# Optimization experiments

Hardware: AMD Instinct MI355X
Metric: run time of the kernel (lower is better)

## Reference

```python
import jax, jax.numpy as jnp
import numpy as np

D = 256  # out_size / d_model
B, S = 8, 4096


def setup_inputs() -> dict:
    key = jax.random.key(0)
    ks = jax.random.split(key, 10)
    std = 1.0 / np.sqrt(D)
    x = jax.random.normal(ks[0], (B, S, D), dtype=jnp.float32)
    Wq = jax.random.uniform(ks[1], (D, D), jnp.float32, -std, std)
    bq = jax.random.uniform(ks[2], (D,), jnp.float32, -std, std)
    Wk = jax.random.uniform(ks[3], (D, D), jnp.float32, -std, std)
    bk = jax.random.uniform(ks[4], (D,), jnp.float32, -std, std)
    Wv = jax.random.uniform(ks[5], (D, D), jnp.float32, -std, std)
    bv = jax.random.uniform(ks[6], (D,), jnp.float32, -std, std)
    Wo = jax.random.uniform(ks[7], (D, D), jnp.float32, -std, std)
    bo = jax.random.uniform(ks[8], (D,), jnp.float32, -std, std)
    cv = jax.random.normal(ks[9], (D, 1), dtype=jnp.float32)
    return {"x": x, "Wq": Wq, "bq": bq, "Wk": Wk, "bk": bk,
            "Wv": Wv, "bv": bv, "Wo": Wo, "bo": bo, "cv": cv}


def reference(x, Wq, bq, Wk, bk, Wv, bv, Wo, bo, cv):
    # Local single-head attention: separate matmul / softmax / matmul
    q = jnp.einsum('bsd,de->bse', x, Wq) + bq
    k = jnp.einsum('bsd,de->bse', x, Wk) + bk
    v = jnp.einsum('bsd,de->bse', x, Wv) + bv
    scale = jnp.sqrt(jnp.asarray(D, dtype=x.dtype))
    scores = jnp.einsum('bqd,bkd->bqk', q, k) / scale  # [B,S,S]
    attn = jax.nn.softmax(scores, axis=-1)
    ctx = jnp.einsum('bqk,bkd->bqd', attn, v)
    logits = jnp.einsum('bsd,de->bse', ctx, Wo) + bo
    # Global context-vector pooling weights (softmax over sequence dim)
    w = jnp.einsum('bsd,dk->bsk', logits, cv)          # [B,S,1]
    nw = jax.nn.softmax(w, axis=1)
    return logits * nw
```

## Files before the change

kernel.cpp:

```cpp
#include <hip/hip_runtime.h>
#include <math.h>
#include <cstddef>
#include <cstdint>

#define B_ 8
#define S_ 4096
#define D_ 256

typedef __attribute__((ext_vector_type(8))) short short8v;
typedef __attribute__((ext_vector_type(4))) short short4v;
typedef __attribute__((ext_vector_type(4))) float float4v;

__device__ __forceinline__ unsigned short f2bf(float f) {
  unsigned u = __float_as_uint(f);
  return (unsigned short)((u + 0x7FFF + ((u >> 16) & 1)) >> 16);
}
__device__ __forceinline__ float bf2f(unsigned short h) {
  return __uint_as_float((unsigned)h << 16);
}
__device__ __forceinline__ unsigned packp(float p) {
  const unsigned short hh = f2bf(p);
  const unsigned short ll = f2bf(p - bf2f(hh));
  return ((unsigned)hh << 16) | (unsigned)ll;
}

__global__ __launch_bounds__(256) void wsplit_kernel(
    const float* __restrict__ Wq, const float* __restrict__ Wk,
    const float* __restrict__ Wv, const float* __restrict__ Wo,
    short* __restrict__ wsp) {
  const int mat = blockIdx.x >> 4;
  const int k0  = (blockIdx.x & 15) << 4;
  const float* W = (mat == 0) ? Wq : (mat == 1) ? Wk : (mat == 2) ? Wv : Wo;
  const int n = threadIdx.x;
  short8v h0, h1, l0, l1;
#pragma unroll
  for (int j = 0; j < 8; ++j) {
    float y = W[(size_t)(k0 + j) * 256 + n];
    unsigned short hh = f2bf(y);
    h0[j] = (short)hh; l0[j] = (short)f2bf(y - bf2f(hh));
    y = W[(size_t)(k0 + 8 + j) * 256 + n];
    hh = f2bf(y);
    h1[j] = (short)hh; l1[j] = (short)f2bf(y - bf2f(hh));
  }
  short* dh = wsp + (size_t)mat * 131072 + (size_t)n * 256 + k0;
  short* dl = dh + 65536;
  *(short8v*)(dh + 0) = h0; *(short8v*)(dh + 8) = h1;
  *(short8v*)(dl + 0) = l0; *(short8v*)(dl + 8) = l1;
}

__global__ __launch_bounds__(256, 2) void proj_qkv_mfma(
    const float* __restrict__ x, const short* __restrict__ wsp,
    const float* __restrict__ bq, const float* __restrict__ bk,
    const float* __restrict__ bvv,
    short* __restrict__ qh, short* __restrict__ ql,
    short* __restrict__ kh, short* __restrict__ kl,
    short* __restrict__ vth, short* __restrict__ vtl) {
  __shared__ __align__(16) short sWh[256 * 40];
  __shared__ __align__(16) short sWl[256 * 40];

  const int t    = threadIdx.x;
  const int w    = t >> 6;
  const int lane = t & 63;
  const int m    = lane & 15;
  const int quad = lane >> 4;
  const size_t r0 = (size_t)blockIdx.x * 64;
  const size_t srow = r0 + 16 * w + m;

  short8v xh[8], xl[8];
#pragma unroll
  for (int kk = 0; kk < 8; ++kk) {
    const float* xp = x + srow * 256 + kk * 32 + quad * 8;
    const float4 a = *(const float4*)xp;
    const float4 b2 = *(const float4*)(xp + 4);
    const float v[8] = {a.x, a.y, a.z, a.w, b2.x, b2.y, b2.z, b2.w};
    short8v h, l;
#pragma unroll
    for (int e = 0; e < 8; ++e) {
      const unsigned short hh = f2bf(v[e]);
      h[e] = (short)hh; l[e] = (short)f2bf(v[e] - bf2f(hh));
    }
    xh[kk] = h; xl[kk] = l;
  }

#pragma unroll
  for (int p = 0; p < 3; ++p) {
    const short* wbase = wsp + (size_t)p * 131072;
    float4v acc[16];
#pragma unroll
    for (int nt = 0; nt < 16; ++nt) acc[nt] = (float4v){0.f, 0.f, 0.f, 0.f};

    for (int kk = 0; kk < 8; ++kk) {
      __syncthreads();
      {
        const short* gh = wbase + (size_t)t * 256 + kk * 32;
        const short* gl = gh + 65536;
#pragma unroll
        for (int j = 0; j < 4; ++j) {
          *(short8v*)&sWh[t * 40 + j * 8] = *(const short8v*)(gh + j * 8);
          *(short8v*)&sWl[t * 40 + j * 8] = *(const short8v*)(gl + j * 8);
        }
      }
      __syncthreads();
#pragma unroll
      for (int nt = 0; nt < 16; ++nt) {
        const short8v wh = *(const short8v*)&sWh[(nt * 16 + m) * 40 + quad * 8];
        const short8v wl = *(const short8v*)&sWl[(nt * 16 + m) * 40 + quad * 8];
        if (p < 2) {
          acc[nt] = __builtin_amdgcn_mfma_f32_16x16x32_bf16(wh, xh[kk], acc[nt], 0, 0, 0);
          acc[nt] = __builtin_amdgcn_mfma_f32_16x16x32_bf16(wh, xl[kk], acc[nt], 0, 0, 0);
          acc[nt] = __builtin_amdgcn_mfma_f32_16x16x32_bf16(wl, xh[kk], acc[nt], 0, 0, 0);
        } else {
          acc[nt] = __builtin_amdgcn_mfma_f32_16x16x32_bf16(xh[kk], wh, acc[nt], 0, 0, 0);
          acc[nt] = __builtin_amdgcn_mfma_f32_16x16x32_bf16(xh[kk], wl, acc[nt], 0, 0, 0);
          acc[nt] = __builtin_amdgcn_mfma_f32_16x16x32_bf16(xl[kk], wh, acc[nt], 0, 0, 0);
        }
      }
    }

    if (p < 2) {
      const float scale = (p == 0) ? 0.0625f : 1.0f;
      short* oh = (p == 0) ? qh : kh;
      short* ol = (p == 0) ? ql : kl;
      const float* bias = (p == 0) ? bq : bk;
#pragma unroll
      for (int nt = 0; nt < 16; ++nt) {
        const float4 bb = *(const float4*)(bias + nt * 16 + quad * 4);
        const float bb4[4] = {bb.x, bb.y, bb.z, bb.w};
        short4v h4, l4;
#pragma unroll
        for (int r = 0; r < 4; ++r) {
          const float y = (acc[nt][r] + bb4[r]) * scale;
          const unsigned short hh = f2bf(y);
          h4[r] = (short)hh; l4[r] = (short)f2bf(y - bf2f(hh));
        }
        *(short4v*)(oh + srow * 256 + nt * 16 + quad * 4) = h4;
        *(short4v*)(ol + srow * 256 + nt * 16 + quad * 4) = l4;
      }
    } else {
      const int bidx = (int)(r0 >> 12);
      const size_t bD = (size_t)bidx * (D_ * (size_t)S_);
      const int sl0 = (int)(r0 & 4095) + 16 * w + quad * 4;
#pragma unroll
      for (int nt = 0; nt < 16; ++nt) {
        const int d = nt * 16 + m;
        const float bn = bvv[d];
        short4v h4, l4;
#pragma unroll
        for (int r = 0; r < 4; ++r) {
          const float y = acc[nt][r] + bn;
          const unsigned short hh = f2bf(y);
          h4[r] = (short)hh; l4[r] = (short)f2bf(y - bf2f(hh));
        }
        *(short4v*)(vth + bD + (size_t)d * S_ + sl0) = h4;
        *(short4v*)(vtl + bD + (size_t)d * S_ + sl0) = l4;
      }
    }
  }
}

__global__ __launch_bounds__(256, 2) void gemm_out_mfma(
    const float* __restrict__ ctx, const short* __restrict__ wsp,
    const float* __restrict__ bo, const float* __restrict__ cv,
    float* __restrict__ out, float* __restrict__ wvec) {
  __shared__ __align__(16) short sWh[256 * 40];
  __shared__ __align__(16) short sWl[256 * 40];

  const int t    = threadIdx.x;
  const int w    = t >> 6;
  const int lane = t & 63;
  const int m    = lane & 15;
  const int quad = lane >> 4;
  const size_t r0 = (size_t)blockIdx.x * 64;
  const size_t srow = r0 + 16 * w + m;
  const short* wbase = wsp + (size_t)3 * 131072;

  short8v ah[8], al[8];
#pragma unroll
  for (int kk = 0; kk < 8; ++kk) {
    const float* xp = ctx + srow * 256 + kk * 32 + quad * 8;
    const float4 a = *(const float4*)xp;
    const float4 b2 = *(const float4*)(xp + 4);
    const float v[8] = {a.x, a.y, a.z, a.w, b2.x, b2.y, b2.z, b2.w};
    short8v h, l;
#pragma unroll
    for (int e = 0; e < 8; ++e) {
      const unsigned short hh = f2bf(v[e]);
      h[e] = (short)hh; l[e] = (short)f2bf(v[e] - bf2f(hh));
    }
    ah[kk] = h; al[kk] = l;
  }

  float4v acc[16];
#pragma unroll
  for (int nt = 0; nt < 16; ++nt) acc[nt] = (float4v){0.f, 0.f, 0.f, 0.f};

  for (int kk = 0; kk < 8; ++kk) {
    __syncthreads();
    {
      const short* gh = wbase + (size_t)t * 256 + kk * 32;
      const short* gl = gh + 65536;
#pragma unroll
      for (int j = 0; j < 4; ++j) {
        *(short8v*)&sWh[t * 40 + j * 8] = *(const short8v*)(gh + j * 8);
        *(short8v*)&sWl[t * 40 + j * 8] = *(const short8v*)(gl + j * 8);
      }
    }
    __syncthreads();
#pragma unroll
    for (int nt = 0; nt < 16; ++nt) {
      const short8v wh = *(const short8v*)&sWh[(nt * 16 + m) * 40 + quad * 8];
      const short8v wl = *(const short8v*)&sWl[(nt * 16 + m) * 40 + quad * 8];
      acc[nt] = __builtin_amdgcn_mfma_f32_16x16x32_bf16(wh, ah[kk], acc[nt], 0, 0, 0);
      acc[nt] = __builtin_amdgcn_mfma_f32_16x16x32_bf16(wh, al[kk], acc[nt], 0, 0, 0);
      acc[nt] = __builtin_amdgcn_mfma_f32_16x16x32_bf16(wl, ah[kk], acc[nt], 0, 0, 0);
    }
  }

  float wp = 0.f;
  float* orow = out + srow * 256;
#pragma unroll
  for (int nt = 0; nt < 16; ++nt) {
    const float4 bb = *(const float4*)(bo + nt * 16 + quad * 4);
    const float4 cc = *(const float4*)(cv + nt * 16 + quad * 4);
    float4 o;
    o.x = acc[nt][0] + bb.x; o.y = acc[nt][1] + bb.y;
    o.z = acc[nt][2] + bb.z; o.w = acc[nt][3] + bb.w;
    wp += o.x * cc.x + o.y * cc.y + o.z * cc.z + o.w * cc.w;
    *(float4*)(orow + nt * 16 + quad * 4) = o;
  }
  wp += __shfl_xor(wp, 16, 64);
  wp += __shfl_xor(wp, 32, 64);
  if (quad == 0) wvec[srow] = wp;
}

__global__ __launch_bounds__(512, 2) void flash_attn_mfma(
    const short* __restrict__ qh, const short* __restrict__ ql,
    const short* __restrict__ kh, const short* __restrict__ kl,
    const short* __restrict__ vth, const short* __restrict__ vtl,
    float* __restrict__ ctx) {
  __shared__ __align__(16) short sK[16896];
  __shared__ __align__(16) short sV[20480];
  __shared__ unsigned int sP[8][16][36];

  const int t    = threadIdx.x;
  const int w    = t >> 6;
  const int lane = t & 63;
  const int m    = lane & 15;
  const int quad = lane >> 4;
  const int q0   = blockIdx.x * 128;
  const int b    = blockIdx.y;
  const size_t sd = (size_t)b * (S_ * (size_t)D_);
  const size_t bD = (size_t)b * (D_ * (size_t)S_);

  short8v aqh[8], aql[8];
  {
    const size_t row = sd + (size_t)(q0 + 16 * w + m) * D_;
#pragma unroll
    for (int kk = 0; kk < 8; ++kk) {
      const size_t off = row + kk * 32 + quad * 8;
      aqh[kk] = *(const short8v*)(qh + off);
      aql[kk] = *(const short8v*)(ql + off);
    }
  }

  short8v ones;
#pragma unroll
  for (int e = 0; e < 8; ++e) ones[e] = (short)0x3F80;

  float4v acc[16];
#pragma unroll
  for (int dt = 0; dt < 16; ++dt) acc[dt] = (float4v){0.f, 0.f, 0.f, 0.f};
  float4v accl = (float4v){0.f, 0.f, 0.f, 0.f};
  float m_i = -INFINITY;

  const int kr0 = t >> 5;
  const int kc0 = (t & 31) << 3;
  const int vd  = t >> 1;
  const int vjh = (t & 1) << 4;

  short8v rKh0, rKh1, rKl0, rKl1;
  short8v rVh0, rVh1, rVl0, rVl1;

  {
    const size_t g0 = sd + (size_t)kr0 * D_ + kc0;
    const size_t g1 = sd + (size_t)(16 + kr0) * D_ + kc0;
    rKh0 = *(const short8v*)(kh + g0);
    rKh1 = *(const short8v*)(kh + g1);
    rKl0 = *(const short8v*)(kl + g0);
    rKl1 = *(const short8v*)(kl + g1);
  }

  for (int jt = 0; jt < 128; ++jt) {
    const int j0 = jt << 5;

    *(short8v*)&sK[kr0 * 264 + kc0]               = rKh0;
    *(short8v*)&sK[(16 + kr0) * 264 + kc0]        = rKh1;
    *(short8v*)&sK[8448 + kr0 * 264 + kc0]        = rKl0;
    *(short8v*)&sK[8448 + (16 + kr0) * 264 + kc0] = rKl1;
    {
      const size_t g = bD + (size_t)vd * S_ + j0 + vjh;
      rVh0 = *(const short8v*)(vth + g);
      rVh1 = *(const short8v*)(vth + g + 8);
      rVl0 = *(const short8v*)(vtl + g);
      rVl1 = *(const short8v*)(vtl + g + 8);
    }
    asm volatile("s_waitcnt lgkmcnt(0)" ::: "memory");
    __builtin_amdgcn_s_barrier();
    asm volatile("" ::: "memory");

    float4v s0 = (float4v){0.f, 0.f, 0.f, 0.f};
    float4v s1 = (float4v){0.f, 0.f, 0.f, 0.f};
    __builtin_amdgcn_s_setprio(1);
#pragma unroll
    for (int kk = 0; kk < 8; ++kk) {
      const int co = kk * 32 + quad * 8;
      const short8v bh0 = *(const short8v*)&sK[m * 264 + co];
      const short8v bl0 = *(const short8v*)&sK[8448 + m * 264 + co];
      const short8v bh1 = *(const short8v*)&sK[(16 + m) * 264 + co];
      const short8v bl1 = *(const short8v*)&sK[8448 + (16 + m) * 264 + co];
      s0 = __builtin_amdgcn_mfma_f32_16x16x32_bf16(bh0, aqh[kk], s0, 0, 0, 0);
      s0 = __builtin_amdgcn_mfma_f32_16x16x32_bf16(bh0, aql[kk], s0, 0, 0, 0);
      s0 = __builtin_amdgcn_mfma_f32_16x16x32_bf16(bl0, aqh[kk], s0, 0, 0, 0);
      s1 = __builtin_amdgcn_mfma_f32_16x16x32_bf16(bh1, aqh[kk], s1, 0, 0, 0);
      s1 = __builtin_amdgcn_mfma_f32_16x16x32_bf16(bh1, aql[kk], s1, 0, 0, 0);
      s1 = __builtin_amdgcn_mfma_f32_16x16x32_bf16(bl1, aqh[kk], s1, 0, 0, 0);
    }
    __builtin_amdgcn_s_setprio(0);

    {
      float mx = fmaxf(fmaxf(fmaxf(s0[0], s0[1]), fmaxf(s0[2], s0[3])),
                       fmaxf(fmaxf(s1[0], s1[1]), fmaxf(s1[2], s1[3])));
      mx = fmaxf(mx, __shfl_xor(mx, 16, 64));
      mx = fmaxf(mx, __shfl_xor(mx, 32, 64));
      if (__any(mx > m_i + 8.0f)) {
        const float mnew = fmaxf(m_i, mx);
        const float alpha = __expf(m_i - mnew);
        m_i = mnew;
        float al[4];
#pragma unroll
        for (int r = 0; r < 4; ++r) al[r] = __shfl(alpha, 20 * quad + r, 64);
#pragma unroll
        for (int dt = 0; dt < 16; ++dt)
#pragma unroll
          for (int r = 0; r < 4; ++r) acc[dt][r] *= al[r];
#pragma unroll
        for (int r = 0; r < 4; ++r) accl[r] *= al[r];
      }
    }

    {
      uint4 w0, w1;
      w0.x = packp(__expf(s0[0] - m_i));
      w0.y = packp(__expf(s0[1] - m_i));
      w0.z = packp(__expf(s0[2] - m_i));
      w0.w = packp(__expf(s0[3] - m_i));
      w1.x = packp(__expf(s1[0] - m_i));
      w1.y = packp(__expf(s1[1] - m_i));
      w1.z = packp(__expf(s1[2] - m_i));
      w1.w = packp(__expf(s1[3] - m_i));
      *(uint4*)&sP[w][m][4 * quad]      = w0;
      *(uint4*)&sP[w][m][16 + 4 * quad] = w1;
    }

    *(short8v*)&sV[vd * 40 + vjh]               = rVh0;
    *(short8v*)&sV[vd * 40 + vjh + 8]           = rVh1;
    *(short8v*)&sV[10240 + vd * 40 + vjh]       = rVl0;
    *(short8v*)&sV[10240 + vd * 40 + vjh + 8]   = rVl1;
    if (jt < 127) {
      const int j0n = j0 + 32;
      const size_t g0 = sd + (size_t)(j0n + kr0) * D_ + kc0;
      const size_t g1 = sd + (size_t)(j0n + 16 + kr0) * D_ + kc0;
      rKh0 = *(const short8v*)(kh + g0);
      rKh1 = *(const short8v*)(kh + g1);
      rKl0 = *(const short8v*)(kl + g0);
      rKl1 = *(const short8v*)(kl + g1);
    }
    asm volatile("s_waitcnt lgkmcnt(0)" ::: "memory");
    __builtin_amdgcn_s_barrier();
    asm volatile("" ::: "memory");

    short8v ph, pl;
    {
      const uint4 pa = *(const uint4*)&sP[w][m][quad * 8];
      const uint4 pb = *(const uint4*)&sP[w][m][quad * 8 + 4];
      ph[0] = (short)(pa.x >> 16); pl[0] = (short)(pa.x & 0xffff);
      ph[1] = (short)(pa.y >> 16); pl[1] = (short)(pa.y & 0xffff);
      ph[2] = (short)(pa.z >> 16); pl[2] = (short)(pa.z & 0xffff);
      ph[3] = (short)(pa.w >> 16); pl[3] = (short)(pa.w & 0xffff);
      ph[4] = (short)(pb.x >> 16); pl[4] = (short)(pb.x & 0xffff);
      ph[5] = (short)(pb.y >> 16); pl[5] = (short)(pb.y & 0xffff);
      ph[6] = (short)(pb.z >> 16); pl[6] = (short)(pb.z & 0xffff);
      ph[7] = (short)(pb.w >> 16); pl[7] = (short)(pb.w & 0xffff);
    }

    __builtin_amdgcn_s_setprio(1);
    accl = __builtin_amdgcn_mfma_f32_16x16x32_bf16(ph, ones, accl, 0, 0, 0);
    accl = __builtin_amdgcn_mfma_f32_16x16x32_bf16(pl, ones, accl, 0, 0, 0);
#pragma unroll
    for (int dt = 0; dt < 16; ++dt) {
      const int vr = (dt * 16 + m) * 40 + quad * 8;
      const short8v bh = *(const short8v*)&sV[vr];
      const short8v bl = *(const short8v*)&sV[10240 + vr];
      acc[dt] = __builtin_amdgcn_mfma_f32_16x16x32_bf16(ph, bh, acc[dt], 0, 0, 0);
      acc[dt] = __builtin_amdgcn_mfma_f32_16x16x32_bf16(ph, bl, acc[dt], 0, 0, 0);
      acc[dt] = __builtin_amdgcn_mfma_f32_16x16x32_bf16(pl, bh, acc[dt], 0, 0, 0);
    }
    __builtin_amdgcn_s_setprio(0);
  }

#pragma unroll
  for (int r = 0; r < 4; ++r) {
    const float inv = 1.0f / accl[r];
    float* cp = ctx + sd + (size_t)(q0 + 16 * w + quad * 4 + r) * D_ + m;
#pragma unroll
    for (int dt = 0; dt < 16; ++dt) cp[dt * 16] = acc[dt][r] * inv;
  }
}

__global__ __launch_bounds__(256) void seq_softmax_kernel(float* __restrict__ w) {
  __shared__ float red[4];
  const int b = blockIdx.x, t = threadIdx.x;
  const int wave = t >> 6, lane = t & 63;
  float* wb = w + (size_t)b * S_;
  float vals[16];
  float mx = -INFINITY;
#pragma unroll
  for (int i = 0; i < 16; ++i) {
    vals[i] = wb[t + (i << 8)];
    mx = fmaxf(mx, vals[i]);
  }
#pragma unroll
  for (int off = 32; off > 0; off >>= 1) mx = fmaxf(mx, __shfl_xor(mx, off, 64));
  if (lane == 0) red[wave] = mx;
  __syncthreads();
  const float M = fmaxf(fmaxf(red[0], red[1]), fmaxf(red[2], red[3]));
  float sum = 0.f;
#pragma unroll
  for (int i = 0; i < 16; ++i) {
    vals[i] = __expf(vals[i] - M);
    sum += vals[i];
  }
#pragma unroll
  for (int off = 32; off > 0; off >>= 1) sum += __shfl_xor(sum, off, 64);
  __syncthreads();
  if (lane == 0) red[wave] = sum;
  __syncthreads();
  const float inv = 1.0f / (red[0] + red[1] + red[2] + red[3]);
#pragma unroll
  for (int i = 0; i < 16; ++i) wb[t + (i << 8)] = vals[i] * inv;
}

__global__ __launch_bounds__(256) void scale_kernel(
    float* __restrict__ out, const float* __restrict__ nw) {
  const size_t g = (size_t)blockIdx.x * 256 + threadIdx.x;
  float4* o4 = (float4*)out;
  float4 vv = o4[g];
  const float sc = nw[g >> 6];
  vv.x *= sc; vv.y *= sc; vv.z *= sc; vv.w *= sc;
  o4[g] = vv;
}

extern "C" void kernel_launch(void* const* d_in, const int* in_sizes, int n_in,
                              void* d_out, int out_size, void* d_ws, size_t ws_size,
                              hipStream_t stream) {
  const float* x  = (const float*)d_in[0];
  const float* Wq = (const float*)d_in[1];
  const float* bq = (const float*)d_in[2];
  const float* Wk = (const float*)d_in[3];
  const float* bk = (const float*)d_in[4];
  const float* Wv = (const float*)d_in[5];
  const float* bv = (const float*)d_in[6];
  const float* Wo = (const float*)d_in[7];
  const float* bo = (const float*)d_in[8];
  const float* cv = (const float*)d_in[9];
  float* out = (float*)d_out;

  const size_t N = (size_t)B_ * S_ * D_;
  short* qh  = (short*)d_ws;
  short* ql  = qh + N;
  short* kh  = ql + N;
  short* kl  = kh + N;
  short* vth = kl + N;
  short* vtl = vth + N;
  float* ctx = (float*)(vtl + N);
  float* w   = ctx + N;
  short* wsp = (short*)(w + (size_t)B_ * S_);

  wsplit_kernel<<<64, 256, 0, stream>>>(Wq, Wk, Wv, Wo, wsp);
  proj_qkv_mfma<<<512, 256, 0, stream>>>(x, wsp, bq, bk, bv,
                                         qh, ql, kh, kl, vth, vtl);
  flash_attn_mfma<<<dim3(32, 8), 512, 0, stream>>>(qh, ql, kh, kl, vth, vtl, ctx);
  gemm_out_mfma<<<512, 256, 0, stream>>>(ctx, wsp, bo, cv, out, w);
  seq_softmax_kernel<<<8, 256, 0, stream>>>(w);
  scale_kernel<<<8192, 256, 0, stream>>>(out, w);
}
```

Measured before the change: 592.6 us.

## Pipeline attention PV, prefetch weights in projections, fuse softmax with scale

The flash-attention loop gains double-buffered V and P tiles, so the P·V MFMAs for the previous tile run while the next tile's scores are computed. The deferred online-softmax rescale is applied after that accumulation. The projection GEMMs move to 512-thread blocks covering 128 rows and register-prefetch the next weight slice before the barrier, reducing how often the weight tiles pass through LDS. The sequence softmax and output scaling are merged into one kernel that recomputes the max and sum per block, which adds redundant reductions but removes a launch and a pass over memory.

```diff
diff --git a/kernel.cpp b/kernel.cpp
--- a/kernel.cpp
+++ b/kernel.cpp
@@ -48,7 +48,7 @@
   *(short8v*)(dl + 0) = l0; *(short8v*)(dl + 8) = l1;
 }
 
-__global__ __launch_bounds__(256, 2) void proj_qkv_mfma(
+__global__ __launch_bounds__(512, 2) void proj_qkv_mfma(
     const float* __restrict__ x, const short* __restrict__ wsp,
     const float* __restrict__ bq, const float* __restrict__ bk,
     const float* __restrict__ bvv,
@@ -63,7 +63,7 @@
   const int lane = t & 63;
   const int m    = lane & 15;
   const int quad = lane >> 4;
-  const size_t r0 = (size_t)blockIdx.x * 64;
+  const size_t r0 = (size_t)blockIdx.x * 128;
   const size_t srow = r0 + 16 * w + m;
 
   short8v xh[8], xl[8];
@@ -82,25 +82,46 @@
     xh[kk] = h; xl[kk] = l;
   }
 
+  const int nr   = t >> 1;
+  const int kh16 = (t & 1) << 4;
+  short8v rh0, rh1, rl0, rl1;
+  {
+    const short* gh = wsp + (size_t)nr * 256 + kh16;
+    const short* gl = gh + 65536;
+    rh0 = *(const short8v*)gh;       rh1 = *(const short8v*)(gh + 8);
+    rl0 = *(const short8v*)gl;       rl1 = *(const short8v*)(gl + 8);
+  }
+
 #pragma unroll
   for (int p = 0; p < 3; ++p) {
-    const short* wbase = wsp + (size_t)p * 131072;
     float4v acc[16];
 #pragma unroll
     for (int nt = 0; nt < 16; ++nt) acc[nt] = (float4v){0.f, 0.f, 0.f, 0.f};
 
     for (int kk = 0; kk < 8; ++kk) {
-      __syncthreads();
+      asm volatile("s_waitcnt lgkmcnt(0)" ::: "memory");
+      __builtin_amdgcn_s_barrier();
+      asm volatile("" ::: "memory");
+      *(short8v*)&sWh[nr * 40 + kh16]     = rh0;
+      *(short8v*)&sWh[nr * 40 + kh16 + 8] = rh1;
+      *(short8v*)&sWl[nr * 40 + kh16]     = rl0;
+      *(short8v*)&sWl[nr * 40 + kh16 + 8] = rl1;
       {
-        const short* gh = wbase + (size_t)t * 256 + kk * 32;
-        const short* gl = gh + 65536;
-#pragma unroll
-        for (int j = 0; j < 4; ++j) {
-          *(short8v*)&sWh[t * 40 + j * 8] = *(const short8v*)(gh + j * 8);
-          *(short8v*)&sWl[t * 40 + j * 8] = *(const short8v*)(gl + j * 8);
+        const int np = (kk < 7) ? p : p + 1;
+        const int nk = (kk < 7) ? kk + 1 : 0;
+        if (np < 3) {
+          const short* gh = wsp + (size_t)np * 131072 +
+                            (size_t)nr * 256 + nk * 32 + kh16;
+          const short* gl = gh + 65536;
+          rh0 = *(const short8v*)gh;   rh1 = *(const short8v*)(gh + 8);
+          rl0 = *(const short8v*)gl;   rl1 = *(const short8v*)(gl + 8);
         }
       }
-      __syncthreads();
+      asm volatile("s_waitcnt lgkmcnt(0)" ::: "memory");
+      __builtin_amdgcn_s_barrier();
+      asm volatile("" ::: "memory");
+
+      __builtin_amdgcn_s_setprio(1);
 #pragma unroll
       for (int nt = 0; nt < 16; ++nt) {
         const short8v wh = *(const short8v*)&sWh[(nt * 16 + m) * 40 + quad * 8];
@@ -115,6 +136,7 @@
           acc[nt] = __builtin_amdgcn_mfma_f32_16x16x32_bf16(xl[kk], wh, acc[nt], 0, 0, 0);
         }
       }
+      __builtin_amdgcn_s_setprio(0);
     }
 
     if (p < 2) {
@@ -158,7 +180,7 @@
   }
 }
 
-__global__ __launch_bounds__(256, 2) void gemm_out_mfma(
+__global__ __launch_bounds__(512, 2) void gemm_out_mfma(
     const float* __restrict__ ctx, const short* __restrict__ wsp,
     const float* __restrict__ bo, const float* __restrict__ cv,
     float* __restrict__ out, float* __restrict__ wvec) {
@@ -170,7 +192,7 @@
   const int lane = t & 63;
   const int m    = lane & 15;
   const int quad = lane >> 4;
-  const size_t r0 = (size_t)blockIdx.x * 64;
+  const size_t r0 = (size_t)blockIdx.x * 128;
   const size_t srow = r0 + 16 * w + m;
   const short* wbase = wsp + (size_t)3 * 131072;
 
@@ -190,22 +212,39 @@
     ah[kk] = h; al[kk] = l;
   }
 
+  const int nr   = t >> 1;
+  const int kh16 = (t & 1) << 4;
+  short8v rh0, rh1, rl0, rl1;
+  {
+    const short* gh = wbase + (size_t)nr * 256 + kh16;
+    const short* gl = gh + 65536;
+    rh0 = *(const short8v*)gh;       rh1 = *(const short8v*)(gh + 8);
+    rl0 = *(const short8v*)gl;       rl1 = *(const short8v*)(gl + 8);
+  }
+
   float4v acc[16];
 #pragma unroll
   for (int nt = 0; nt < 16; ++nt) acc[nt] = (float4v){0.f, 0.f, 0.f, 0.f};
 
   for (int kk = 0; kk < 8; ++kk) {
-    __syncthreads();
-    {
-      const short* gh = wbase + (size_t)t * 256 + kk * 32;
+    asm volatile("s_waitcnt lgkmcnt(0)" ::: "memory");
+    __builtin_amdgcn_s_barrier();
+    asm volatile("" ::: "memory");
+    *(short8v*)&sWh[nr * 40 + kh16]     = rh0;
+    *(short8v*)&sWh[nr * 40 + kh16 + 8] = rh1;
+    *(short8v*)&sWl[nr * 40 + kh16]     = rl0;
+    *(short8v*)&sWl[nr * 40 + kh16 + 8] = rl1;
+    if (kk < 7) {
+      const short* gh = wbase + (size_t)nr * 256 + (kk + 1) * 32 + kh16;
       const short* gl = gh + 65536;
-#pragma unroll
-      for (int j = 0; j < 4; ++j) {
-        *(short8v*)&sWh[t * 40 + j * 8] = *(const short8v*)(gh + j * 8);
-        *(short8v*)&sWl[t * 40 + j * 8] = *(const short8v*)(gl + j * 8);
-      }
-    }
-    __syncthreads();
+      rh0 = *(const short8v*)gh;   rh1 = *(const short8v*)(gh + 8);
+      rl0 = *(const short8v*)gl;   rl1 = *(const short8v*)(gl + 8);
+    }
+    asm volatile("s_waitcnt lgkmcnt(0)" ::: "memory");
+    __builtin_amdgcn_s_barrier();
+    asm volatile("" ::: "memory");
+
+    __builtin_amdgcn_s_setprio(1);
 #pragma unroll
     for (int nt = 0; nt < 16; ++nt) {
       const short8v wh = *(const short8v*)&sWh[(nt * 16 + m) * 40 + quad * 8];
@@ -214,6 +253,7 @@
       acc[nt] = __builtin_amdgcn_mfma_f32_16x16x32_bf16(wh, al[kk], acc[nt], 0, 0, 0);
       acc[nt] = __builtin_amdgcn_mfma_f32_16x16x32_bf16(wl, ah[kk], acc[nt], 0, 0, 0);
     }
+    __builtin_amdgcn_s_setprio(0);
   }
 
   float wp = 0.f;
@@ -239,8 +279,8 @@
     const short* __restrict__ vth, const short* __restrict__ vtl,
     float* __restrict__ ctx) {
   __shared__ __align__(16) short sK[16896];
-  __shared__ __align__(16) short sV[20480];
-  __shared__ unsigned int sP[8][16][36];
+  __shared__ __align__(16) short sV[2][20480];
+  __shared__ __align__(16) unsigned int sP[2][8][16][36];
 
   const int t    = threadIdx.x;
   const int w    = t >> 6;
@@ -291,7 +331,9 @@
   }
 
   for (int jt = 0; jt < 128; ++jt) {
-    const int j0 = jt << 5;
+    const int j0  = jt << 5;
+    const int cur = jt & 1;
+    const int old = cur ^ 1;
 
     *(short8v*)&sK[kr0 * 264 + kc0]               = rKh0;
     *(short8v*)&sK[(16 + kr0) * 264 + kc0]        = rKh1;
@@ -327,6 +369,8 @@
     }
     __builtin_amdgcn_s_setprio(0);
 
+    float alpha_p = 1.0f;
+    bool fired = false;
     {
       float mx = fmaxf(fmaxf(fmaxf(s0[0], s0[1]), fmaxf(s0[2], s0[3])),
                        fmaxf(fmaxf(s1[0], s1[1]), fmaxf(s1[2], s1[3])));
@@ -334,17 +378,9 @@
       mx = fmaxf(mx, __shfl_xor(mx, 32, 64));
       if (__any(mx > m_i + 8.0f)) {
         const float mnew = fmaxf(m_i, mx);
-        const float alpha = __expf(m_i - mnew);
+        alpha_p = __expf(m_i - mnew);
         m_i = mnew;
-        float al[4];
-#pragma unroll
-        for (int r = 0; r < 4; ++r) al[r] = __shfl(alpha, 20 * quad + r, 64);
-#pragma unroll
-        for (int dt = 0; dt < 16; ++dt)
-#pragma unroll
-          for (int r = 0; r < 4; ++r) acc[dt][r] *= al[r];
-#pragma unroll
-        for (int r = 0; r < 4; ++r) accl[r] *= al[r];
+        fired = true;
       }
     }
 
@@ -358,14 +394,59 @@
       w1.y = packp(__expf(s1[1] - m_i));
       w1.z = packp(__expf(s1[2] - m_i));
       w1.w = packp(__expf(s1[3] - m_i));
-      *(uint4*)&sP[w][m][4 * quad]      = w0;
-      *(uint4*)&sP[w][m][16 + 4 * quad] = w1;
-    }
-
-    *(short8v*)&sV[vd * 40 + vjh]               = rVh0;
-    *(short8v*)&sV[vd * 40 + vjh + 8]           = rVh1;
-    *(short8v*)&sV[10240 + vd * 40 + vjh]       = rVl0;
-    *(short8v*)&sV[10240 + vd * 40 + vjh + 8]   = rVl1;
+      *(uint4*)&sP[cur][w][m][4 * quad]      = w0;
+      *(uint4*)&sP[cur][w][m][16 + 4 * quad] = w1;
+    }
+
+    if (jt > 0) {
+      short8v ph, pl;
+      {
+        const uint4 pa = *(const uint4*)&sP[old][w][m][quad * 8];
+        const uint4 pb = *(const uint4*)&sP[old][w][m][quad * 8 + 4];
+        ph[0] = (short)(pa.x >> 16); pl[0] = (short)(pa.x & 0xffff);
+        ph[1] = (short)(pa.y >> 16); pl[1] = (short)(pa.y & 0xffff);
+        ph[2] = (short)(pa.z >> 16); pl[2] = (short)(pa.z & 0xffff);
+        ph[3] = (short)(pa.w >> 16); pl[3] = (short)(pa.w & 0xffff);
+        ph[4] = (short)(pb.x >> 16); pl[4] = (short)(pb.x & 0xffff);
+        ph[5] = (short)(pb.y >> 16); pl[5] = (short)(pb.y & 0xffff);
+        ph[6] = (short)(pb.z >> 16); pl[6] = (short)(pb.z & 0xffff);
+        ph[7] = (short)(pb.w >> 16); pl[7] = (short)(pb.w & 0xffff);
+      }
+      const short* sVo = &sV[old][0];
+      __builtin_amdgcn_s_setprio(1);
+      accl = __builtin_amdgcn_mfma_f32_16x16x32_bf16(ph, ones, accl, 0, 0, 0);
+      accl = __builtin_amdgcn_mfma_f32_16x16x32_bf16(pl, ones, accl, 0, 0, 0);
+#pragma unroll
+      for (int dt = 0; dt < 16; ++dt) {
+        const int vr = (dt * 16 + m) * 40 + quad * 8;
+        const short8v bh = *(const short8v*)&sVo[vr];
+        const short8v bl = *(const short8v*)&sVo[10240 + vr];
+        acc[dt] = __builtin_amdgcn_mfma_f32_16x16x32_bf16(ph, bh, acc[dt], 0, 0, 0);
+        acc[dt] = __builtin_amdgcn_mfma_f32_16x16x32_bf16(ph, bl, acc[dt], 0, 0, 0);
+        acc[dt] = __builtin_amdgcn_mfma_f32_16x16x32_bf16(pl, bh, acc[dt], 0, 0, 0);
+      }
+      __builtin_amdgcn_s_setprio(0);
+    }
+
+    if (fired) {
+      float al[4];
+#pragma unroll
+      for (int r = 0; r < 4; ++r) al[r] = __shfl(alpha_p, 20 * quad + r, 64);
+#pragma unroll
+      for (int dt = 0; dt < 16; ++dt)
+#pragma unroll
+        for (int r = 0; r < 4; ++r) acc[dt][r] *= al[r];
+#pragma unroll
+      for (int r = 0; r < 4; ++r) accl[r] *= al[r];
+    }
+
+    {
+      short* sVc = &sV[cur][0];
+      *(short8v*)&sVc[vd * 40 + vjh]             = rVh0;
+      *(short8v*)&sVc[vd * 40 + vjh + 8]         = rVh1;
+      *(short8v*)&sVc[10240 + vd * 40 + vjh]     = rVl0;
+      *(short8v*)&sVc[10240 + vd * 40 + vjh + 8] = rVl1;
+    }
     if (jt < 127) {
       const int j0n = j0 + 32;
       const size_t g0 = sd + (size_t)(j0n + kr0) * D_ + kc0;
@@ -378,11 +459,13 @@
     asm volatile("s_waitcnt lgkmcnt(0)" ::: "memory");
     __builtin_amdgcn_s_barrier();
     asm volatile("" ::: "memory");
-
+  }
+
+  {
     short8v ph, pl;
     {
-      const uint4 pa = *(const uint4*)&sP[w][m][quad * 8];
-      const uint4 pb = *(const uint4*)&sP[w][m][quad * 8 + 4];
+      const uint4 pa = *(const uint4*)&sP[1][w][m][quad * 8];
+      const uint4 pb = *(const uint4*)&sP[1][w][m][quad * 8 + 4];
       ph[0] = (short)(pa.x >> 16); pl[0] = (short)(pa.x & 0xffff);
       ph[1] = (short)(pa.y >> 16); pl[1] = (short)(pa.y & 0xffff);
       ph[2] = (short)(pa.z >> 16); pl[2] = (short)(pa.z & 0xffff);
@@ -392,20 +475,18 @@
       ph[6] = (short)(pb.z >> 16); pl[6] = (short)(pb.z & 0xffff);
       ph[7] = (short)(pb.w >> 16); pl[7] = (short)(pb.w & 0xffff);
     }
-
-    __builtin_amdgcn_s_setprio(1);
+    const short* sVo = &sV[1][0];
     accl = __builtin_amdgcn_mfma_f32_16x16x32_bf16(ph, ones, accl, 0, 0, 0);
     accl = __builtin_amdgcn_mfma_f32_16x16x32_bf16(pl, ones, accl, 0, 0, 0);
 #pragma unroll
     for (int dt = 0; dt < 16; ++dt) {
       const int vr = (dt * 16 + m) * 40 + quad * 8;
-      const short8v bh = *(const short8v*)&sV[vr];
-      const short8v bl = *(const short8v*)&sV[10240 + vr];
+      const short8v bh = *(const short8v*)&sVo[vr];
+      const short8v bl = *(const short8v*)&sVo[10240 + vr];
       acc[dt] = __builtin_amdgcn_mfma_f32_16x16x32_bf16(ph, bh, acc[dt], 0, 0, 0);
       acc[dt] = __builtin_amdgcn_mfma_f32_16x16x32_bf16(ph, bl, acc[dt], 0, 0, 0);
       acc[dt] = __builtin_amdgcn_mfma_f32_16x16x32_bf16(pl, bh, acc[dt], 0, 0, 0);
     }
-    __builtin_amdgcn_s_setprio(0);
   }
 
 #pragma unroll
@@ -417,18 +498,17 @@
   }
 }
 
-__global__ __launch_bounds__(256) void seq_softmax_kernel(float* __restrict__ w) {
+__global__ __launch_bounds__(256) void softmax_scale_kernel(
+    float* __restrict__ out, const float* __restrict__ wv) {
   __shared__ float red[4];
-  const int b = blockIdx.x, t = threadIdx.x;
+  const int t = threadIdx.x;
   const int wave = t >> 6, lane = t & 63;
-  float* wb = w + (size_t)b * S_;
-  float vals[16];
+  const int b = blockIdx.x >> 8;
+  const float* wb = wv + (size_t)b * S_;
+
   float mx = -INFINITY;
 #pragma unroll
-  for (int i = 0; i < 16; ++i) {
-    vals[i] = wb[t + (i << 8)];
-    mx = fmaxf(mx, vals[i]);
-  }
+  for (int i = 0; i < 16; ++i) mx = fmaxf(mx, wb[t + (i << 8)]);
 #pragma unroll
   for (int off = 32; off > 0; off >>= 1) mx = fmaxf(mx, __shfl_xor(mx, off, 64));
   if (lane == 0) red[wave] = mx;
@@ -436,28 +516,24 @@
   const float M = fmaxf(fmaxf(red[0], red[1]), fmaxf(red[2], red[3]));
   float sum = 0.f;
 #pragma unroll
-  for (int i = 0; i < 16; ++i) {
-    vals[i] = __expf(vals[i] - M);
-    sum += vals[i];
-  }
+  for (int i = 0; i < 16; ++i) sum += __expf(wb[t + (i << 8)] - M);
 #pragma unroll
   for (int off = 32; off > 0; off >>= 1) sum += __shfl_xor(sum, off, 64);
   __syncthreads();
   if (lane == 0) red[wave] = sum;
   __syncthreads();
   const float inv = 1.0f / (red[0] + red[1] + red[2] + red[3]);
-#pragma unroll
-  for (int i = 0; i < 16; ++i) wb[t + (i << 8)] = vals[i] * inv;
-}
-
-__global__ __launch_bounds__(256) void scale_kernel(
-    float* __restrict__ out, const float* __restrict__ nw) {
-  const size_t g = (size_t)blockIdx.x * 256 + threadIdx.x;
+
   float4* o4 = (float4*)out;
-  float4 vv = o4[g];
-  const float sc = nw[g >> 6];
-  vv.x *= sc; vv.y *= sc; vv.z *= sc; vv.w *= sc;
-  o4[g] = vv;
+  const size_t g0 = (size_t)blockIdx.x * 1024 + t;
+#pragma unroll
+  for (int i = 0; i < 4; ++i) {
+    const size_t g = g0 + (size_t)(i << 8);
+    const float sc = __expf(wv[g >> 6] - M) * inv;
+    float4 vv = o4[g];
+    vv.x *= sc; vv.y *= sc; vv.z *= sc; vv.w *= sc;
+    o4[g] = vv;
+  }
 }
 
 extern "C" void kernel_launch(void* const* d_in, const int* in_sizes, int n_in,
@@ -487,10 +563,9 @@
   short* wsp = (short*)(w + (size_t)B_ * S_);
 
   wsplit_kernel<<<64, 256, 0, stream>>>(Wq, Wk, Wv, Wo, wsp);
-  proj_qkv_mfma<<<512, 256, 0, stream>>>(x, wsp, bq, bk, bv,
+  proj_qkv_mfma<<<256, 512, 0, stream>>>(x, wsp, bq, bk, bv,
                                          qh, ql, kh, kl, vth, vtl);
   flash_attn_mfma<<<dim3(32, 8), 512, 0, stream>>>(qh, ql, kh, kl, vth, vtl, ctx);
-  gemm_out_mfma<<<512, 256, 0, stream>>>(ctx, wsp, bo, cv, out, w);
-  seq_softmax_kernel<<<8, 256, 0, stream>>>(w);
-  scale_kernel<<<8192, 256, 0, stream>>>(out, w);
-}
+  gemm_out_mfma<<<256, 512, 0, stream>>>(ctx, wsp, bo, cv, out, w);
+  softmax_scale_kernel<<<2048, 256, 0, stream>>>(out, w);
+}
```

After: 598.5 us. No clear change (+1.0%).
